# Kernel tuning notes

Measured on AMD Instinct MI355X. Metric: run time of the kernel, lower is better.

## Reference

```python
import jax, jax.numpy as jnp
import numpy as np
from jax import lax

ALPHA = 0.1
HIDDEN_DIM = 512


def setup_inputs() -> dict:
    key = jax.random.key(0)
    ks = jax.random.split(key, 8)
    B, T, I, H, O, R = 64, 1024, 128, 512, 512, 2
    x = jax.random.normal(ks[0], (B, T, I), dtype=jnp.float32)
    h0 = jnp.zeros((B, H), dtype=jnp.float32)
    Wxh = jax.random.normal(ks[1], (H, I), dtype=jnp.float32) / np.sqrt(I)
    bxh = jax.random.normal(ks[2], (H,), dtype=jnp.float32) * 0.01
    U = jax.random.normal(ks[3], (H, R), dtype=jnp.float32) / np.sqrt(H)
    V = jax.random.normal(ks[4], (H, R), dtype=jnp.float32) / np.sqrt(H)
    Why = jax.random.normal(ks[5], (O, H), dtype=jnp.float32) / np.sqrt(H)
    bhy = jax.random.normal(ks[6], (O,), dtype=jnp.float32) * 0.01
    return {"x": x, "h0": h0, "Wxh": Wxh, "bxh": bxh, "U": U, "V": V,
            "Why": Why, "bhy": bhy}


def reference(x, h0, Wxh, bxh, U, V, Why, bhy):
    # x: (B,T,I); precompute the input projection for all timesteps at once
    xproj = jnp.einsum('bti,hi->bth', x, Wxh) + bxh  # (B,T,H)

    def step(h, xp_t):
        # low-rank recurrent map: h @ V @ U.T / hidden_dim
        pre = xp_t + (h @ V) @ U.T / HIDDEN_DIM  # (B,H)
        h_new = (1.0 - ALPHA) * h + ALPHA * jnp.tanh(pre)
        return h_new, h_new

    _, hs = lax.scan(step, h0, jnp.swapaxes(xproj, 0, 1))  # hs: (T,B,H)
    h_all = jnp.swapaxes(hs, 0, 1)  # (B,T,H)
    y = jnp.einsum('bth,oh->bto', h_all, Why) + bhy  # (B,T,O)
    return y, h_all
```

## Files before the change

kernel.cpp:

```cpp
#include <hip/hip_runtime.h>
#include <hip/hip_bf16.h>
#include <cstdint>

#define B_ 64
#define T_ 1024
#define I_ 128
#define H_ 512
#define O_ 512

#define CHUNK_L 64
#define NCHUNK (T_ / CHUNK_L)
#define WARM_ 160

typedef short bf16x8 __attribute__((ext_vector_type(8)));
typedef float f32x4 __attribute__((ext_vector_type(4)));

typedef const __attribute__((address_space(1))) void* gptr_t;
typedef __attribute__((address_space(3))) void* lptr_t;

__device__ __forceinline__ unsigned short f2bf(float f) {
    unsigned int u = __float_as_uint(f);
    u += 0x7fffu + ((u >> 16) & 1u);
    return (unsigned short)(u >> 16);
}
__device__ __forceinline__ float bf2f(unsigned short b) {
    return __uint_as_float(((unsigned int)b) << 16);
}
__device__ __forceinline__ float fast_tanh(float x) {
    float e = __builtin_amdgcn_exp2f(x * 2.8853900817779268f);
    return 1.0f - 2.0f * __builtin_amdgcn_rcpf(e + 1.0f);
}

template <int CTRL>
__device__ __forceinline__ float dpp_add(float v) {
    int t = __builtin_amdgcn_update_dpp(0, __float_as_int(v), CTRL, 0xf, 0xf, true);
    return v + __int_as_float(t);
}
__device__ __forceinline__ float wave_sum64(float v) {
    v = dpp_add<0x111>(v);
    v = dpp_add<0x112>(v);
    v = dpp_add<0x114>(v);
    v = dpp_add<0x118>(v);
    v = dpp_add<0x142>(v);
    v = dpp_add<0x143>(v);
    return __uint_as_float(__builtin_amdgcn_readlane(__float_as_uint(v), 63));
}

__global__ __launch_bounds__(256)
void cast_f32_bf16(const float* __restrict__ s, unsigned short* __restrict__ d, int n) {
    int i = (blockIdx.x * 256 + threadIdx.x) * 4;
    if (i >= n) return;
    float4 v = *(const float4*)(s + i);
    ushort4 o;
    o.x = f2bf(v.x); o.y = f2bf(v.y); o.z = f2bf(v.z); o.w = f2bf(v.w);
    *(ushort4*)(d + i) = o;
}

template <bool STORE_BF16>
__global__ __launch_bounds__(256)
void gemm_bt(const unsigned short* __restrict__ A,
             const unsigned short* __restrict__ Bm,
             const float* __restrict__ bias,
             void* __restrict__ Cout,
             int M, int N, int K) {
    __shared__ unsigned short As[128 * 32];
    __shared__ unsigned short Bs[128 * 32];

    const int tid  = threadIdx.x;
    const int lane = tid & 63;
    const int w    = tid >> 6;
    const int wm   = (w >> 1) * 64;
    const int wn   = (w & 1) * 64;
    const int nblk = N >> 7;
    const int bm   = (int)(blockIdx.x / nblk) << 7;
    const int bn   = (int)(blockIdx.x % nblk) << 7;

    f32x4 acc[4][4] = {};

    const int srow = tid >> 2;
    const int scol = (tid & 3) << 3;
    const unsigned short* gA0 = A  + (size_t)(bm + srow) * K + scol;
    const unsigned short* gA1 = A  + (size_t)(bm + 64 + srow) * K + scol;
    const unsigned short* gB0 = Bm + (size_t)(bn + srow) * K + scol;
    const unsigned short* gB1 = Bm + (size_t)(bn + 64 + srow) * K + scol;

    unsigned short* ldsA0 = As + w * 512;
    unsigned short* ldsA1 = As + 2048 + w * 512;
    unsigned short* ldsB0 = Bs + w * 512;
    unsigned short* ldsB1 = Bs + 2048 + w * 512;

    const int frow = lane & 15;
    const int fk   = (lane >> 4) << 3;

    for (int kt = 0; kt < K; kt += 32) {
        __syncthreads();
        __builtin_amdgcn_global_load_lds((gptr_t)(gA0 + kt), (lptr_t)ldsA0, 16, 0, 0);
        __builtin_amdgcn_global_load_lds((gptr_t)(gA1 + kt), (lptr_t)ldsA1, 16, 0, 0);
        __builtin_amdgcn_global_load_lds((gptr_t)(gB0 + kt), (lptr_t)ldsB0, 16, 0, 0);
        __builtin_amdgcn_global_load_lds((gptr_t)(gB1 + kt), (lptr_t)ldsB1, 16, 0, 0);
        __syncthreads();

        bf16x8 af[4], bf[4];
#pragma unroll
        for (int mt = 0; mt < 4; ++mt)
            af[mt] = *(const bf16x8*)(As + (wm + mt * 16 + frow) * 32 + fk);
#pragma unroll
        for (int nt = 0; nt < 4; ++nt)
            bf[nt] = *(const bf16x8*)(Bs + (wn + nt * 16 + frow) * 32 + fk);
#pragma unroll
        for (int mt = 0; mt < 4; ++mt)
#pragma unroll
            for (int nt = 0; nt < 4; ++nt)
                acc[mt][nt] = __builtin_amdgcn_mfma_f32_16x16x32_bf16(
                    af[mt], bf[nt], acc[mt][nt], 0, 0, 0);
    }

    const int c_col = lane & 15;
    const int c_row = (lane >> 4) << 2;
#pragma unroll
    for (int nt = 0; nt < 4; ++nt) {
        const int gn = bn + wn + nt * 16 + c_col;
        const float bv = bias[gn];
#pragma unroll
        for (int mt = 0; mt < 4; ++mt) {
            const int gm0 = bm + wm + mt * 16 + c_row;
#pragma unroll
            for (int r = 0; r < 4; ++r) {
                float v = acc[mt][nt][r] + bv;
                size_t idx = (size_t)(gm0 + r) * N + gn;
                if (STORE_BF16) ((unsigned short*)Cout)[idx] = f2bf(v);
                else            ((float*)Cout)[idx] = v;
            }
        }
    }
}

__global__ __launch_bounds__(64)
void scan_kernel(const unsigned short* __restrict__ xproj,
                 const float* __restrict__ h0,
                 const float* __restrict__ U,
                 const float* __restrict__ V,
                 float* __restrict__ hall_f32,
                 unsigned short* __restrict__ hall_bf) {
    const int blk = blockIdx.x;
    const int b = blk / NCHUNK;
    const int c = blk % NCHUNK;
    const int t_start = c * CHUNK_L;
    const int t0 = (t_start - WARM_ > 0) ? (t_start - WARM_) : 0;
    const int t_end = t_start + CHUNK_L;

    const int lane = threadIdx.x;
    const int hbase = lane * 8;

    float h[8], V0[8], V1[8], U0[8], U1[8];
#pragma unroll
    for (int j = 0; j < 8; ++j) {
        V0[j] = V[(hbase + j) * 2 + 0];
        V1[j] = V[(hbase + j) * 2 + 1];
        U0[j] = U[(hbase + j) * 2 + 0];
        U1[j] = U[(hbase + j) * 2 + 1];
    }
    if (t0 == 0) {
#pragma unroll
        for (int j = 0; j < 8; ++j) h[j] = h0[b * H_ + hbase + j];
    } else {
#pragma unroll
        for (int j = 0; j < 8; ++j) h[j] = 0.f;
    }

    const unsigned short* xp_ptr = xproj + ((size_t)b * T_ + t0) * H_ + hbase;
    float* ho = hall_f32 + (size_t)b * T_ * H_ + hbase;
    unsigned short* hb = hall_bf + (size_t)b * T_ * H_ + hbase;

    const float inv_h = 1.0f / (float)H_;
    uint4 xcur = *(const uint4*)xp_ptr;

    float s0 = 0.f, s1 = 0.f;
#pragma unroll
    for (int j = 0; j < 8; ++j) { s0 += h[j] * V0[j]; s1 += h[j] * V1[j]; }
    s0 = wave_sum64(s0);
    s1 = wave_sum64(s1);

    int t = t0;

#define SCAN_STEP(DO_STORE)                                                    \
    {                                                                          \
        uint4 xnext = make_uint4(0u, 0u, 0u, 0u);                              \
        if (t + 1 < t_end)                                                     \
            xnext = *(const uint4*)(xp_ptr + (size_t)(t + 1 - t0) * H_);       \
        float xp[8];                                                           \
        {                                                                      \
            unsigned int uu[4] = {xcur.x, xcur.y, xcur.z, xcur.w};             \
            _Pragma("unroll")                                                  \
            for (int q = 0; q < 4; ++q) {                                      \
                xp[2 * q + 0] = bf2f((unsigned short)(uu[q] & 0xffffu));       \
                xp[2 * q + 1] = bf2f((unsigned short)(uu[q] >> 16));           \
            }                                                                  \
        }                                                                      \
        const float c0 = s0 * inv_h, c1 = s1 * inv_h;                          \
        float g[8];                                                            \
        _Pragma("unroll")                                                      \
        for (int j = 0; j < 8; ++j)                                            \
            g[j] = fast_tanh(xp[j] + c0 * U0[j] + c1 * U1[j]);                 \
        _Pragma("unroll")                                                      \
        for (int j = 0; j < 8; ++j)                                            \
            h[j] = 0.9f * h[j] + 0.1f * g[j];                                  \
        float p0a = 0.f, p0b = 0.f, p1a = 0.f, p1b = 0.f;                      \
        _Pragma("unroll")                                                      \
        for (int j = 0; j < 4; ++j) {                                          \
            p0a += g[j] * V0[j];       p0b += g[j + 4] * V0[j + 4];            \
            p1a += g[j] * V1[j];       p1b += g[j + 4] * V1[j + 4];            \
        }                                                                      \
        float r0 = wave_sum64(p0a + p0b);                                      \
        float r1 = wave_sum64(p1a + p1b);                                      \
        s0 = 0.9f * s0 + 0.1f * r0;                                            \
        s1 = 0.9f * s1 + 0.1f * r1;                                            \
        if (DO_STORE) {                                                        \
            float4 v0 = make_float4(h[0], h[1], h[2], h[3]);                   \
            float4 v1 = make_float4(h[4], h[5], h[6], h[7]);                   \
            *(float4*)(ho + (size_t)t * H_ + 0) = v0;                          \
            *(float4*)(ho + (size_t)t * H_ + 4) = v1;                          \
            uint4 pb;                                                          \
            pb.x = ((unsigned int)f2bf(h[1]) << 16) | f2bf(h[0]);              \
            pb.y = ((unsigned int)f2bf(h[3]) << 16) | f2bf(h[2]);              \
            pb.z = ((unsigned int)f2bf(h[5]) << 16) | f2bf(h[4]);              \
            pb.w = ((unsigned int)f2bf(h[7]) << 16) | f2bf(h[6]);              \
            *(uint4*)(hb + (size_t)t * H_) = pb;                               \
        }                                                                      \
        xcur = xnext;                                                          \
    }

    for (; t < t_start; ++t) SCAN_STEP(false)
    for (; t < t_end; ++t) SCAN_STEP(true)
#undef SCAN_STEP
}

extern "C" void kernel_launch(void* const* d_in, const int* in_sizes, int n_in,
                              void* d_out, int out_size, void* d_ws, size_t ws_size,
                              hipStream_t stream) {
    const float* x   = (const float*)d_in[0];
    const float* h0  = (const float*)d_in[1];
    const float* Wxh = (const float*)d_in[2];
    const float* bxh = (const float*)d_in[3];
    const float* U   = (const float*)d_in[4];
    const float* V   = (const float*)d_in[5];
    const float* Why = (const float*)d_in[6];
    const float* bhy = (const float*)d_in[7];

    float* y    = (float*)d_out;
    float* hall = y + (size_t)B_ * T_ * O_;

    unsigned short* x_bf    = (unsigned short*)d_ws;
    unsigned short* Wxh_bf  = x_bf + (size_t)B_ * T_ * I_;
    unsigned short* Why_bf  = Wxh_bf + (size_t)H_ * I_;
    unsigned short* xp_bf   = Why_bf + (size_t)O_ * H_;
    unsigned short* hall_bf = xp_bf + (size_t)B_ * T_ * H_;

    cast_f32_bf16<<<(B_ * T_ * I_) / 1024, 256, 0, stream>>>(x, x_bf, B_ * T_ * I_);
    cast_f32_bf16<<<(H_ * I_) / 1024, 256, 0, stream>>>(Wxh, Wxh_bf, H_ * I_);
    cast_f32_bf16<<<(O_ * H_) / 1024, 256, 0, stream>>>(Why, Why_bf, O_ * H_);

    gemm_bt<true><<<dim3((B_ * T_ / 128) * (H_ / 128)), 256, 0, stream>>>(
        x_bf, Wxh_bf, bxh, xp_bf, B_ * T_, H_, I_);

    scan_kernel<<<B_ * NCHUNK, 64, 0, stream>>>(xp_bf, h0, U, V, hall, hall_bf);

    gemm_bt<false><<<dim3((B_ * T_ / 128) * (O_ / 128)), 256, 0, stream>>>(
        hall_bf, Why_bf, bhy, y, B_ * T_, O_, H_);
}
```

Measured before the change: 518.2 us.

## Shorten scan warmup, prefetch xproj four steps ahead, fold 1/H into V, merge casts

Cuts the per-chunk warmup of the chunked scan from 160 to 96 steps, which removes redundant recurrence work but relies on the decay (0.9^96) to keep chunk-boundary error small. Replaces the single-step xproj prefetch with a four-register rotating prefetch to hide global load latency in the serial loop. Folds the 1/H scaling into V and skips the initial reduction when the state is zero. Also merges three cast launches into one kernel to cut launch overhead.

```diff
diff --git a/kernel.cpp b/kernel.cpp
--- a/kernel.cpp
+++ b/kernel.cpp
@@ -10,7 +10,7 @@
 
 #define CHUNK_L 64
 #define NCHUNK (T_ / CHUNK_L)
-#define WARM_ 160
+#define WARM_ 96
 
 typedef short bf16x8 __attribute__((ext_vector_type(8)));
 typedef float f32x4 __attribute__((ext_vector_type(4)));
@@ -46,14 +46,25 @@
     return __uint_as_float(__builtin_amdgcn_readlane(__float_as_uint(v), 63));
 }
 
+#define NX_ (B_ * T_ * I_)
+#define NW_ (H_ * I_)
+#define NY_ (O_ * H_)
+
 __global__ __launch_bounds__(256)
-void cast_f32_bf16(const float* __restrict__ s, unsigned short* __restrict__ d, int n) {
-    int i = (blockIdx.x * 256 + threadIdx.x) * 4;
-    if (i >= n) return;
-    float4 v = *(const float4*)(s + i);
+void cast_all(const float* __restrict__ x, const float* __restrict__ Wxh,
+              const float* __restrict__ Why, unsigned short* __restrict__ xb,
+              unsigned short* __restrict__ wb, unsigned short* __restrict__ yb) {
+    int i4 = (blockIdx.x * 256 + threadIdx.x) * 4;
+    const float* s;
+    unsigned short* d;
+    int off;
+    if (i4 < NX_)             { s = x;   d = xb; off = i4; }
+    else if (i4 < NX_ + NW_)  { s = Wxh; d = wb; off = i4 - NX_; }
+    else                      { s = Why; d = yb; off = i4 - NX_ - NW_; }
+    float4 v = *(const float4*)(s + off);
     ushort4 o;
     o.x = f2bf(v.x); o.y = f2bf(v.y); o.z = f2bf(v.z); o.w = f2bf(v.w);
-    *(ushort4*)(d + i) = o;
+    *(ushort4*)(d + off) = o;
 }
 
 template <bool STORE_BF16>
@@ -147,16 +158,18 @@
     const int c = blk % NCHUNK;
     const int t_start = c * CHUNK_L;
     const int t0 = (t_start - WARM_ > 0) ? (t_start - WARM_) : 0;
-    const int t_end = t_start + CHUNK_L;
+    const int nwarm = t_start - t0;
+    const int NT = nwarm + CHUNK_L;
 
     const int lane = threadIdx.x;
     const int hbase = lane * 8;
 
+    const float inv_h = 1.0f / (float)H_;
     float h[8], V0[8], V1[8], U0[8], U1[8];
 #pragma unroll
     for (int j = 0; j < 8; ++j) {
-        V0[j] = V[(hbase + j) * 2 + 0];
-        V1[j] = V[(hbase + j) * 2 + 1];
+        V0[j] = V[(hbase + j) * 2 + 0] * inv_h;
+        V1[j] = V[(hbase + j) * 2 + 1] * inv_h;
         U0[j] = U[(hbase + j) * 2 + 0];
         U1[j] = U[(hbase + j) * 2 + 1];
     }
@@ -168,40 +181,44 @@
         for (int j = 0; j < 8; ++j) h[j] = 0.f;
     }
 
-    const unsigned short* xp_ptr = xproj + ((size_t)b * T_ + t0) * H_ + hbase;
+    const unsigned short* xp = xproj + ((size_t)b * T_ + t0) * H_ + hbase;
     float* ho = hall_f32 + (size_t)b * T_ * H_ + hbase;
     unsigned short* hb = hall_bf + (size_t)b * T_ * H_ + hbase;
 
-    const float inv_h = 1.0f / (float)H_;
-    uint4 xcur = *(const uint4*)xp_ptr;
-
     float s0 = 0.f, s1 = 0.f;
-#pragma unroll
-    for (int j = 0; j < 8; ++j) { s0 += h[j] * V0[j]; s1 += h[j] * V1[j]; }
-    s0 = wave_sum64(s0);
-    s1 = wave_sum64(s1);
-
-    int t = t0;
-
-#define SCAN_STEP(DO_STORE)                                                    \
+    if (t0 == 0) {
+        float a0 = 0.f, a1 = 0.f;
+#pragma unroll
+        for (int j = 0; j < 8; ++j) { a0 += h[j] * V0[j]; a1 += h[j] * V1[j]; }
+        s0 = wave_sum64(a0);
+        s1 = wave_sum64(a1);
+    }
+
+    uint4 xq0, xq1, xq2, xq3;
+#define LOADX(DST, IDX)                                                        \
+    if ((IDX) < NT) DST = *(const uint4*)(xp + (size_t)(IDX) * H_);
+    xq0 = *(const uint4*)xp;
+    LOADX(xq1, 1)
+    LOADX(xq2, 2)
+    LOADX(xq3, 3)
+
+#define SCAN_SLOT(REG, IDX, DO_STORE)                                          \
     {                                                                          \
-        uint4 xnext = make_uint4(0u, 0u, 0u, 0u);                              \
-        if (t + 1 < t_end)                                                     \
-            xnext = *(const uint4*)(xp_ptr + (size_t)(t + 1 - t0) * H_);       \
-        float xp[8];                                                           \
+        uint4 xc = REG;                                                        \
+        LOADX(REG, (IDX) + 4)                                                  \
+        float xp8[8];                                                          \
         {                                                                      \
-            unsigned int uu[4] = {xcur.x, xcur.y, xcur.z, xcur.w};             \
+            unsigned int uu[4] = {xc.x, xc.y, xc.z, xc.w};                     \
             _Pragma("unroll")                                                  \
             for (int q = 0; q < 4; ++q) {                                      \
-                xp[2 * q + 0] = bf2f((unsigned short)(uu[q] & 0xffffu));       \
-                xp[2 * q + 1] = bf2f((unsigned short)(uu[q] >> 16));           \
+                xp8[2 * q + 0] = bf2f((unsigned short)(uu[q] & 0xffffu));      \
+                xp8[2 * q + 1] = bf2f((unsigned short)(uu[q] >> 16));          \
             }                                                                  \
         }                                                                      \
-        const float c0 = s0 * inv_h, c1 = s1 * inv_h;                          \
         float g[8];                                                            \
         _Pragma("unroll")                                                      \
         for (int j = 0; j < 8; ++j)                                            \
-            g[j] = fast_tanh(xp[j] + c0 * U0[j] + c1 * U1[j]);                 \
+            g[j] = fast_tanh(xp8[j] + s0 * U0[j] + s1 * U1[j]);                \
         _Pragma("unroll")                                                      \
         for (int j = 0; j < 8; ++j)                                            \
             h[j] = 0.9f * h[j] + 0.1f * g[j];                                  \
@@ -216,23 +233,35 @@
         s0 = 0.9f * s0 + 0.1f * r0;                                            \
         s1 = 0.9f * s1 + 0.1f * r1;                                            \
         if (DO_STORE) {                                                        \
+            const size_t tt = (size_t)(t0 + (IDX));                            \
             float4 v0 = make_float4(h[0], h[1], h[2], h[3]);                   \
             float4 v1 = make_float4(h[4], h[5], h[6], h[7]);                   \
-            *(float4*)(ho + (size_t)t * H_ + 0) = v0;                          \
-            *(float4*)(ho + (size_t)t * H_ + 4) = v1;                          \
+            *(float4*)(ho + tt * H_ + 0) = v0;                                 \
+            *(float4*)(ho + tt * H_ + 4) = v1;                                 \
             uint4 pb;                                                          \
             pb.x = ((unsigned int)f2bf(h[1]) << 16) | f2bf(h[0]);              \
             pb.y = ((unsigned int)f2bf(h[3]) << 16) | f2bf(h[2]);              \
             pb.z = ((unsigned int)f2bf(h[5]) << 16) | f2bf(h[4]);              \
             pb.w = ((unsigned int)f2bf(h[7]) << 16) | f2bf(h[6]);              \
-            *(uint4*)(hb + (size_t)t * H_) = pb;                               \
+            *(uint4*)(hb + tt * H_) = pb;                                      \
         }                                                                      \
-        xcur = xnext;                                                          \
-    }
-
-    for (; t < t_start; ++t) SCAN_STEP(false)
-    for (; t < t_end; ++t) SCAN_STEP(true)
-#undef SCAN_STEP
+    }
+
+    int I = 0;
+    for (; I < nwarm; I += 4) {
+        SCAN_SLOT(xq0, I + 0, false)
+        SCAN_SLOT(xq1, I + 1, false)
+        SCAN_SLOT(xq2, I + 2, false)
+        SCAN_SLOT(xq3, I + 3, false)
+    }
+    for (; I < NT; I += 4) {
+        SCAN_SLOT(xq0, I + 0, true)
+        SCAN_SLOT(xq1, I + 1, true)
+        SCAN_SLOT(xq2, I + 2, true)
+        SCAN_SLOT(xq3, I + 3, true)
+    }
+#undef SCAN_SLOT
+#undef LOADX
 }
 
 extern "C" void kernel_launch(void* const* d_in, const int* in_sizes, int n_in,
@@ -256,9 +285,8 @@
     unsigned short* xp_bf   = Why_bf + (size_t)O_ * H_;
     unsigned short* hall_bf = xp_bf + (size_t)B_ * T_ * H_;
 
-    cast_f32_bf16<<<(B_ * T_ * I_) / 1024, 256, 0, stream>>>(x, x_bf, B_ * T_ * I_);
-    cast_f32_bf16<<<(H_ * I_) / 1024, 256, 0, stream>>>(Wxh, Wxh_bf, H_ * I_);
-    cast_f32_bf16<<<(O_ * H_) / 1024, 256, 0, stream>>>(Why, Why_bf, O_ * H_);
+    cast_all<<<(NX_ + NW_ + NY_) / 1024, 256, 0, stream>>>(
+        x, Wxh, Why, x_bf, Wxh_bf, Why_bf);
 
     gemm_bt<true><<<dim3((B_ * T_ / 128) * (H_ / 128)), 256, 0, stream>>>(
         x_bf, Wxh_bf, bxh, xp_bf, B_ * T_, H_, I_);
```

New measurement: 466.7 us. 1.11x faster.
